# Kernel tuning notes

Hardware: AMD Instinct MI355X
Metric: run time of the kernel (lower is better)

## Reference

```python
import jax, jax.numpy as jnp
import numpy as np

NUM_ITERATIONS = 3  # matches init kwarg num_iterations
B, R, CIN, COUT, K = 32, 2048, 64, 64, 16


def squash(s):
    # squash along the last (capsule-vector) axis, as in the torch module
    sq = jnp.sum(s * s, axis=-1, keepdims=True)
    return (sq / (1.0 + sq)) * s / jnp.sqrt(sq)


def setup_inputs() -> dict:
    key = jax.random.key(0)
    k1, k2 = jax.random.split(key)
    x = jax.random.normal(k1, (B, R, CIN), dtype=jnp.float32)
    route_weights = jax.random.normal(k2, (K, R, CIN, COUT), dtype=jnp.float32) * 0.05
    return {"x": x, "route_weights": route_weights}


def reference(x, route_weights):
    # priors[k,b,r,o] = sum_c x[b,r,c] * W[k,r,c,o]   -> [K, B, R, COUT]
    priors = jnp.einsum('brc,krco->kbro', x, route_weights)
    logits = jnp.zeros(priors.shape[:3] + (1,), dtype=priors.dtype)  # [K,B,R,1]
    outputs = None
    for i in range(NUM_ITERATIONS):
        probs = jax.nn.softmax(logits, axis=2)  # softmax over route nodes (torch dim=2)
        outputs = squash(jnp.sum(probs * priors, axis=2, keepdims=True))  # [K,B,1,COUT]
        if i != NUM_ITERATIONS - 1:
            logits = logits + jnp.sum(priors * outputs, axis=-1, keepdims=True)
    return outputs[:, :, 0, :]  # [K, B, COUT]
```

## Files before the change

kernel.cpp:

```cpp
#include <hip/hip_runtime.h>
#include <hip/hip_bf16.h>
#include <stdint.h>

#define NB 32
#define NR 2048
#define NC 64
#define NO 64
#define NK 16

using bf16x8 = __attribute__((ext_vector_type(8))) short;
using f32x4  = __attribute__((ext_vector_type(4))) float;

__device__ __forceinline__ uint32_t f2bf(float f) {
  uint32_t u = __builtin_bit_cast(uint32_t, f);
  return (u + 0x7fffu + ((u >> 16) & 1u)) >> 16;
}
__device__ __forceinline__ uint32_t packbf2(float lo, float hi) {
  return f2bf(lo) | (f2bf(hi) << 16);
}

__device__ __forceinline__ void gload_lds16(const float* g, float* l) {
  __builtin_amdgcn_global_load_lds(
      (const __attribute__((address_space(1))) void*)g,
      (__attribute__((address_space(3))) void*)l, 16, 0, 0);
}

__global__ __launch_bounds__(256) void make_xbf(const float* __restrict__ x,
                                                ushort* __restrict__ xbf) {
  __shared__ float tile[32][72];
  const int r = blockIdx.x, t = threadIdx.x;
  {
    const int b = t >> 3, c0 = (t & 7) << 3;
    const float* xp = x + ((size_t)b * NR + r) * NC + c0;
    *(float4*)&tile[b][c0] = *(const float4*)xp;
    *(float4*)&tile[b][c0 + 4] = *(const float4*)(xp + 4);
  }
  __syncthreads();
  {
    const int ks = t >> 7, mt = (t >> 6) & 1, l = t & 63;
    const int b = mt * 16 + (l & 15);
    const int cb = ks * 32 + (l >> 4) * 8;
    uint4 uv;
    uv.x = packbf2(tile[b][cb + 0], tile[b][cb + 1]);
    uv.y = packbf2(tile[b][cb + 2], tile[b][cb + 3]);
    uv.z = packbf2(tile[b][cb + 4], tile[b][cb + 5]);
    uv.w = packbf2(tile[b][cb + 6], tile[b][cb + 7]);
    *(uint4*)(xbf + (size_t)r * 2048 + t * 8) = uv;
  }
}

__global__ __launch_bounds__(256, 2) void priors_gemm(const ushort* __restrict__ xbf,
                                                      const float* __restrict__ W,
                                                      ushort* __restrict__ priors) {
  __shared__ float ldsW[2][4][2048];
  const int w = threadIdx.x >> 6, lane = threadIdx.x & 63;
  const int g = lane >> 4, col = lane & 15;
  const int kq = blockIdx.x & 3, rblk = blockIdx.x >> 2;
  const int k = kq * 4 + w;

  f32x4 acc[2][4];

  auto stage = [&](int rr, int ks, int buf) {
    const float* src = W + ((size_t)(k * NR + rblk * 8 + rr)) * 4096 + ks * 2048 + lane * 4;
    float* dst = &ldsW[buf][w][0] + lane * 4;
#pragma unroll
    for (int i = 0; i < 8; ++i) gload_lds16(src + i * 256, dst + i * 256);
  };

  auto compute = [&](int rr, int ks, int buf) {
    const float* pw = &ldsW[buf][w][0];
    const size_t r = rblk * 8 + rr;
    bf16x8 af0 = *(const bf16x8*)(xbf + ((r * 2 + ks) * 2 + 0) * 512 + lane * 8);
    bf16x8 af1 = *(const bf16x8*)(xbf + ((r * 2 + ks) * 2 + 1) * 512 + lane * 8);
#pragma unroll
    for (int nt = 0; nt < 4; ++nt) {
      float f[8];
#pragma unroll
      for (int e = 0; e < 8; ++e) f[e] = pw[(g * 8 + e) * 64 + nt * 16 + col];
      uint4 uv;
      uv.x = packbf2(f[0], f[1]);
      uv.y = packbf2(f[2], f[3]);
      uv.z = packbf2(f[4], f[5]);
      uv.w = packbf2(f[6], f[7]);
      bf16x8 bfr = __builtin_bit_cast(bf16x8, uv);
      acc[0][nt] = __builtin_amdgcn_mfma_f32_16x16x32_bf16(af0, bfr, acc[0][nt], 0, 0, 0);
      acc[1][nt] = __builtin_amdgcn_mfma_f32_16x16x32_bf16(af1, bfr, acc[1][nt], 0, 0, 0);
    }
  };

  auto epilogue = [&](int rr, int buf) {
    ushort* ep = (ushort*)&ldsW[buf][w][0];
#pragma unroll
    for (int mt = 0; mt < 2; ++mt)
#pragma unroll
      for (int nt = 0; nt < 4; ++nt)
#pragma unroll
        for (int reg = 0; reg < 4; ++reg)
          ep[(mt * 16 + g * 4 + reg) * 64 + nt * 16 + col] = (ushort)f2bf(acc[mt][nt][reg]);
    ushort* pp = priors + ((size_t)(k * NR + rblk * 8 + rr)) * 2048;
#pragma unroll
    for (int i = 0; i < 4; ++i) {
      uint4 v = *(const uint4*)(ep + lane * 8 + i * 512);
      *(uint4*)(pp + lane * 8 + i * 512) = v;
    }
  };

  stage(0, 0, 0);
  __syncthreads();
  for (int ti = 0; ti < 8; ++ti) {
#pragma unroll
    for (int mt = 0; mt < 2; ++mt)
#pragma unroll
      for (int nt = 0; nt < 4; ++nt) acc[mt][nt] = f32x4{0.f, 0.f, 0.f, 0.f};
    stage(ti, 1, 1);
    compute(ti, 0, 0);
    __syncthreads();
    if (ti < 7) stage(ti + 1, 0, 0);
    compute(ti, 1, 1);
    epilogue(ti, 1);
    __syncthreads();
  }
}

template <int PASS>
__global__ __launch_bounds__(256) void routing(const __hip_bfloat16* __restrict__ priors,
                                               float* __restrict__ Abuf,
                                               const float* __restrict__ o_prev,
                                               float* __restrict__ o_out) {
  __shared__ float o_lds[64];
  __shared__ float red_num[4][8][8];
  __shared__ float red_den[4];
  const int kb = blockIdx.x;
  const int k = kb >> 5, b = kb & 31;
  const int tid = threadIdx.x, w = tid >> 6, lane = tid & 63;
  const int g = lane >> 3, sl = lane & 7;
  const int rsub = w * 8 + g;
  const __hip_bfloat16* pbase = priors + (size_t)k * NR * NB * NO + (size_t)b * NO;
  float* ab = Abuf + (size_t)kb * NR;

  if (PASS == 1) {
    float sum[8];
#pragma unroll
    for (int j = 0; j < 8; ++j) sum[j] = 0.f;
    for (int it = 0; it < NR / 32; ++it) {
      const int r = it * 32 + rsub;
      uint4 pv = *(const uint4*)(pbase + (size_t)r * (NB * NO) + sl * 8);
      sum[0] += __builtin_bit_cast(float, pv.x << 16);
      sum[1] += __builtin_bit_cast(float, pv.x & 0xffff0000u);
      sum[2] += __builtin_bit_cast(float, pv.y << 16);
      sum[3] += __builtin_bit_cast(float, pv.y & 0xffff0000u);
      sum[4] += __builtin_bit_cast(float, pv.z << 16);
      sum[5] += __builtin_bit_cast(float, pv.z & 0xffff0000u);
      sum[6] += __builtin_bit_cast(float, pv.w << 16);
      sum[7] += __builtin_bit_cast(float, pv.w & 0xffff0000u);
    }
#pragma unroll
    for (int m = 8; m < 64; m <<= 1)
#pragma unroll
      for (int j = 0; j < 8; ++j) sum[j] += __shfl_xor(sum[j], m, 64);
    if (lane < 8) {
#pragma unroll
      for (int j = 0; j < 8; ++j) red_num[w][lane][j] = sum[j];
    }
    __syncthreads();
    if (tid < 64) {
      const int s_ = tid >> 3, j_ = tid & 7;
      float sv = (red_num[0][s_][j_] + red_num[1][s_][j_] +
                  red_num[2][s_][j_] + red_num[3][s_][j_]) * (1.f / (float)NR);
      float sq = sv * sv;
#pragma unroll
      for (int m = 1; m < 64; m <<= 1) sq += __shfl_xor(sq, m, 64);
      o_lds[tid] = (sq / (1.f + sq)) * rsqrtf(sq) * sv;
    }
    __syncthreads();
  } else {
    if (tid < 64) o_lds[tid] = o_prev[kb * 64 + tid];
    __syncthreads();
  }

  float os[8];
#pragma unroll
  for (int j = 0; j < 8; ++j) os[j] = o_lds[sl * 8 + j];

  float num[8];
#pragma unroll
  for (int j = 0; j < 8; ++j) num[j] = 0.f;
  float den = 0.f;

  for (int it = 0; it < NR / 32; ++it) {
    const int r = it * 32 + rsub;
    uint4 pv = *(const uint4*)(pbase + (size_t)r * (NB * NO) + sl * 8);
    float f[8];
    f[0] = __builtin_bit_cast(float, pv.x << 16);
    f[1] = __builtin_bit_cast(float, pv.x & 0xffff0000u);
    f[2] = __builtin_bit_cast(float, pv.y << 16);
    f[3] = __builtin_bit_cast(float, pv.y & 0xffff0000u);
    f[4] = __builtin_bit_cast(float, pv.z << 16);
    f[5] = __builtin_bit_cast(float, pv.z & 0xffff0000u);
    f[6] = __builtin_bit_cast(float, pv.w << 16);
    f[7] = __builtin_bit_cast(float, pv.w & 0xffff0000u);

    float d = 0.f;
#pragma unroll
    for (int j = 0; j < 8; ++j) d = fmaf(f[j], os[j], d);
#pragma unroll
    for (int m = 1; m < 8; m <<= 1) d += __shfl_xor(d, m, 64);

    float lg;
    if (PASS == 1) {
      lg = d;
      if (sl == 0) ab[r] = d;
    } else {
      lg = d + ab[r];
    }
    float e = __expf(lg);
    den += e;
#pragma unroll
    for (int j = 0; j < 8; ++j) num[j] = fmaf(e, f[j], num[j]);
  }

#pragma unroll
  for (int m = 8; m < 64; m <<= 1) {
    den += __shfl_xor(den, m, 64);
#pragma unroll
    for (int j = 0; j < 8; ++j) num[j] += __shfl_xor(num[j], m, 64);
  }
  if (lane < 8) {
#pragma unroll
    for (int j = 0; j < 8; ++j) red_num[w][lane][j] = num[j];
    if (lane == 0) red_den[w] = den;
  }
  __syncthreads();

  if (tid < 64) {
    const int s_ = tid >> 3, j_ = tid & 7;
    float nm = red_num[0][s_][j_] + red_num[1][s_][j_] + red_num[2][s_][j_] + red_num[3][s_][j_];
    float dn = red_den[0] + red_den[1] + red_den[2] + red_den[3];
    float sv = nm / dn;
    float sq = sv * sv;
#pragma unroll
    for (int m = 1; m < 64; m <<= 1) sq += __shfl_xor(sq, m, 64);
    float ov = (sq / (1.f + sq)) * rsqrtf(sq) * sv;
    o_out[kb * 64 + tid] = ov;
  }
}

extern "C" void kernel_launch(void* const* d_in, const int* in_sizes, int n_in,
                              void* d_out, int out_size, void* d_ws, size_t ws_size,
                              hipStream_t stream) {
  const float* x = (const float*)d_in[0];
  const float* W = (const float*)d_in[1];
  float* out = (float*)d_out;
  char* ws = (char*)d_ws;

  size_t off = 0;
  ushort* xbf = (ushort*)(ws + off);               off += (size_t)NR * 2048 * 2;
  ushort* priors = (ushort*)(ws + off);            off += (size_t)NK * NR * NB * NO * 2;
  float* o1 = (float*)(ws + off);                  off += (size_t)NK * NB * NO * 4;
  float* Abuf = (float*)(ws + off);                off += (size_t)NK * NB * NR * 4;

  make_xbf<<<NR, 256, 0, stream>>>(x, xbf);
  priors_gemm<<<(NR / 8) * (NK / 4), 256, 0, stream>>>(xbf, W, priors);
  routing<1><<<NK * NB, 256, 0, stream>>>((const __hip_bfloat16*)priors, Abuf, nullptr, o1);
  routing<2><<<NK * NB, 256, 0, stream>>>((const __hip_bfloat16*)priors, Abuf, o1, out);
}
```

Measured before the change: 240.7 us.

## Restructure priors GEMM to one (k,r) tile per wave with direct W loads

The priors GEMM drops the LDS double-buffered staging of W through global_load_lds and the 8-row loop per block. Each wave now handles a single (k, r) pair, loading W straight into registers in a layout that puts W in the A operand and x in the B operand of the MFMA. The make_xbf permutation is changed to match, and the epilogue uses a padded LDS tile with packed bf16 conversion. This aims to cut LDS traffic and sync overhead and to raise occupancy through a much larger grid, at the cost of less load pipelining and possibly less coalesced strided W reads.

```diff
diff --git a/kernel.cpp b/kernel.cpp
--- a/kernel.cpp
+++ b/kernel.cpp
@@ -18,11 +18,12 @@
 __device__ __forceinline__ uint32_t packbf2(float lo, float hi) {
   return f2bf(lo) | (f2bf(hi) << 16);
 }
-
-__device__ __forceinline__ void gload_lds16(const float* g, float* l) {
-  __builtin_amdgcn_global_load_lds(
-      (const __attribute__((address_space(1))) void*)g,
-      (__attribute__((address_space(3))) void*)l, 16, 0, 0);
+__device__ __forceinline__ uint32_t cvtpk2(float lo, float hi) {
+  float2 v; v.x = lo; v.y = hi;
+  __hip_bfloat162 h = __float22bfloat162_rn(v);
+  uint32_t r;
+  __builtin_memcpy(&r, &h, 4);
+  return r;
 }
 
 __global__ __launch_bounds__(256) void make_xbf(const float* __restrict__ x,
@@ -37,88 +38,82 @@
   }
   __syncthreads();
   {
-    const int ks = t >> 7, mt = (t >> 6) & 1, l = t & 63;
-    const int b = mt * 16 + (l & 15);
-    const int cb = ks * 32 + (l >> 4) * 8;
+    const int ks = t >> 7, bt = (t >> 6) & 1, l = t & 63;
+    const int kgrp = l >> 4;
+    const int b = bt * 16 + (l & 15);
+    const int cb = ks * 32 + kgrp;
     uint4 uv;
-    uv.x = packbf2(tile[b][cb + 0], tile[b][cb + 1]);
-    uv.y = packbf2(tile[b][cb + 2], tile[b][cb + 3]);
-    uv.z = packbf2(tile[b][cb + 4], tile[b][cb + 5]);
-    uv.w = packbf2(tile[b][cb + 6], tile[b][cb + 7]);
+    uv.x = packbf2(tile[b][cb + 0], tile[b][cb + 4]);
+    uv.y = packbf2(tile[b][cb + 8], tile[b][cb + 12]);
+    uv.z = packbf2(tile[b][cb + 16], tile[b][cb + 20]);
+    uv.w = packbf2(tile[b][cb + 24], tile[b][cb + 28]);
     *(uint4*)(xbf + (size_t)r * 2048 + t * 8) = uv;
   }
 }
 
-__global__ __launch_bounds__(256, 2) void priors_gemm(const ushort* __restrict__ xbf,
-                                                      const float* __restrict__ W,
-                                                      ushort* __restrict__ priors) {
-  __shared__ float ldsW[2][4][2048];
+__global__ __launch_bounds__(256) void priors_gemm(const ushort* __restrict__ xbf,
+                                                   const float* __restrict__ W,
+                                                   ushort* __restrict__ priors) {
+  __shared__ ushort ldsE[4][32 * 72];
   const int w = threadIdx.x >> 6, lane = threadIdx.x & 63;
-  const int g = lane >> 4, col = lane & 15;
-  const int kq = blockIdx.x & 3, rblk = blockIdx.x >> 2;
-  const int k = kq * 4 + w;
-
-  f32x4 acc[2][4];
-
-  auto stage = [&](int rr, int ks, int buf) {
-    const float* src = W + ((size_t)(k * NR + rblk * 8 + rr)) * 4096 + ks * 2048 + lane * 4;
-    float* dst = &ldsW[buf][w][0] + lane * 4;
-#pragma unroll
-    for (int i = 0; i < 8; ++i) gload_lds16(src + i * 256, dst + i * 256);
-  };
-
-  auto compute = [&](int rr, int ks, int buf) {
-    const float* pw = &ldsW[buf][w][0];
-    const size_t r = rblk * 8 + rr;
-    bf16x8 af0 = *(const bf16x8*)(xbf + ((r * 2 + ks) * 2 + 0) * 512 + lane * 8);
-    bf16x8 af1 = *(const bf16x8*)(xbf + ((r * 2 + ks) * 2 + 1) * 512 + lane * 8);
-#pragma unroll
-    for (int nt = 0; nt < 4; ++nt) {
-      float f[8];
-#pragma unroll
-      for (int e = 0; e < 8; ++e) f[e] = pw[(g * 8 + e) * 64 + nt * 16 + col];
+  const int kgrp = lane >> 4, col = lane & 15;
+  const int task = blockIdx.x * 4 + w;
+  const int k = task & 15, r = task >> 4;
+  const float* wbase = W + ((size_t)(k * NR + r)) * 4096;
+  const ushort* xb = xbf + (size_t)r * 2048;
+
+  bf16x8 xfrag[2][2];
+#pragma unroll
+  for (int ks = 0; ks < 2; ++ks)
+#pragma unroll
+    for (int bt = 0; bt < 2; ++bt)
+      xfrag[ks][bt] = *(const bf16x8*)(xb + (ks * 2 + bt) * 512 + lane * 8);
+
+  f32x4 acc[4][2];
+#pragma unroll
+  for (int ot = 0; ot < 4; ++ot)
+#pragma unroll
+    for (int bt = 0; bt < 2; ++bt) acc[ot][bt] = f32x4{0.f, 0.f, 0.f, 0.f};
+
+#pragma unroll
+  for (int ks = 0; ks < 2; ++ks) {
+    float w32[4][8];
+#pragma unroll
+    for (int e = 0; e < 8; ++e) {
+      const float* src = wbase + (ks * 32 + e * 4 + kgrp) * 64 + col;
+#pragma unroll
+      for (int ot = 0; ot < 4; ++ot) w32[ot][e] = src[ot * 16];
+    }
+#pragma unroll
+    for (int ot = 0; ot < 4; ++ot) {
       uint4 uv;
-      uv.x = packbf2(f[0], f[1]);
-      uv.y = packbf2(f[2], f[3]);
-      uv.z = packbf2(f[4], f[5]);
-      uv.w = packbf2(f[6], f[7]);
-      bf16x8 bfr = __builtin_bit_cast(bf16x8, uv);
-      acc[0][nt] = __builtin_amdgcn_mfma_f32_16x16x32_bf16(af0, bfr, acc[0][nt], 0, 0, 0);
-      acc[1][nt] = __builtin_amdgcn_mfma_f32_16x16x32_bf16(af1, bfr, acc[1][nt], 0, 0, 0);
-    }
-  };
-
-  auto epilogue = [&](int rr, int buf) {
-    ushort* ep = (ushort*)&ldsW[buf][w][0];
-#pragma unroll
-    for (int mt = 0; mt < 2; ++mt)
-#pragma unroll
-      for (int nt = 0; nt < 4; ++nt)
-#pragma unroll
-        for (int reg = 0; reg < 4; ++reg)
-          ep[(mt * 16 + g * 4 + reg) * 64 + nt * 16 + col] = (ushort)f2bf(acc[mt][nt][reg]);
-    ushort* pp = priors + ((size_t)(k * NR + rblk * 8 + rr)) * 2048;
-#pragma unroll
-    for (int i = 0; i < 4; ++i) {
-      uint4 v = *(const uint4*)(ep + lane * 8 + i * 512);
-      *(uint4*)(pp + lane * 8 + i * 512) = v;
-    }
-  };
-
-  stage(0, 0, 0);
-  __syncthreads();
-  for (int ti = 0; ti < 8; ++ti) {
-#pragma unroll
-    for (int mt = 0; mt < 2; ++mt)
-#pragma unroll
-      for (int nt = 0; nt < 4; ++nt) acc[mt][nt] = f32x4{0.f, 0.f, 0.f, 0.f};
-    stage(ti, 1, 1);
-    compute(ti, 0, 0);
-    __syncthreads();
-    if (ti < 7) stage(ti + 1, 0, 0);
-    compute(ti, 1, 1);
-    epilogue(ti, 1);
-    __syncthreads();
+      uv.x = cvtpk2(w32[ot][0], w32[ot][1]);
+      uv.y = cvtpk2(w32[ot][2], w32[ot][3]);
+      uv.z = cvtpk2(w32[ot][4], w32[ot][5]);
+      uv.w = cvtpk2(w32[ot][6], w32[ot][7]);
+      bf16x8 af = __builtin_bit_cast(bf16x8, uv);
+      acc[ot][0] = __builtin_amdgcn_mfma_f32_16x16x32_bf16(af, xfrag[ks][0], acc[ot][0], 0, 0, 0);
+      acc[ot][1] = __builtin_amdgcn_mfma_f32_16x16x32_bf16(af, xfrag[ks][1], acc[ot][1], 0, 0, 0);
+    }
+  }
+
+  ushort* ep = &ldsE[w][0];
+#pragma unroll
+  for (int ot = 0; ot < 4; ++ot)
+#pragma unroll
+    for (int bt = 0; bt < 2; ++bt)
+#pragma unroll
+      for (int pr = 0; pr < 2; ++pr) {
+        uint32_t u = cvtpk2(acc[ot][bt][pr * 2], acc[ot][bt][pr * 2 + 1]);
+        const int b = bt * 16 + col, o = ot * 16 + kgrp * 4 + pr * 2;
+        *(uint32_t*)(&ep[b * 72 + o]) = u;
+      }
+  ushort* pp = priors + ((size_t)(k * NR + r)) * 2048;
+#pragma unroll
+  for (int i = 0; i < 4; ++i) {
+    const int row = (lane >> 3) + i * 8, cc = (lane & 7) * 8;
+    uint4 v = *(const uint4*)(&ep[row * 72 + cc]);
+    *(uint4*)(pp + row * 64 + cc) = v;
   }
 }
 
@@ -260,7 +255,7 @@
   float* Abuf = (float*)(ws + off);                off += (size_t)NK * NB * NR * 4;
 
   make_xbf<<<NR, 256, 0, stream>>>(x, xbf);
-  priors_gemm<<<(NR / 8) * (NK / 4), 256, 0, stream>>>(xbf, W, priors);
+  priors_gemm<<<(NR * NK) / 4, 256, 0, stream>>>(xbf, W, priors);
   routing<1><<<NK * NB, 256, 0, stream>>>((const __hip_bfloat16*)priors, Abuf, nullptr, o1);
   routing<2><<<NK * NB, 256, 0, stream>>>((const __hip_bfloat16*)priors, Abuf, o1, out);
 }
```

After: 219.6 us. 8.8% less time.
